# Kernel optimization log

Hardware: AMD Instinct MI355X
Metric: run time of the kernel (lower is better)

The kernel has to match this reference:

```python
import jax, jax.numpy as jnp
import numpy as np
import math

N_EMBD = 384
N_HEAD = 6
HEAD_DIM = N_EMBD // N_HEAD  # 64
EPS = 1e-5


def apply_rotary_emb(x, cos, sin):
    # x: [B, T, H, D]; cos/sin: [1, T, 1, D//2]
    d = x.shape[3] // 2
    x1, x2 = x[..., :d], x[..., d:]
    y1 = x1 * cos + x2 * sin
    y2 = -x1 * sin + x2 * cos
    return jnp.concatenate([y1, y2], axis=3).astype(x.dtype)


def rms_norm(x):
    # no learned gain, eps inside the sqrt's argument as in the torch code
    return x * jax.lax.rsqrt(jnp.mean(x * x, axis=-1, keepdims=True) + EPS)


def setup_inputs() -> dict:
    key = jax.random.key(0)
    ks = jax.random.split(key, 7)
    B, T = 8, 2048
    x = jax.random.normal(ks[0], (B, T, N_EMBD), dtype=jnp.float32)
    scale = 1.0 / math.sqrt(N_EMBD)
    Wq = jax.random.normal(ks[1], (N_EMBD, N_EMBD), dtype=jnp.float32) * scale
    Wk = jax.random.normal(ks[2], (N_EMBD, N_EMBD), dtype=jnp.float32) * scale
    Wv = jax.random.normal(ks[3], (N_EMBD, N_EMBD), dtype=jnp.float32) * scale
    Wo = jax.random.normal(ks[4], (N_EMBD, N_EMBD), dtype=jnp.float32) * scale
    # RoPE tables: true cos/sin of position*inv_freq
    half = HEAD_DIM // 2
    inv_freq = 1.0 / (10000.0 ** (jnp.arange(half, dtype=jnp.float32) / half))
    t = jnp.arange(T, dtype=jnp.float32)
    freqs = t[:, None] * inv_freq[None, :]  # [T, half]
    cos = jnp.cos(freqs)[None, :, None, :]  # [1, T, 1, half]
    sin = jnp.sin(freqs)[None, :, None, :]
    return {"x": x, "Wq": Wq, "Wk": Wk, "Wv": Wv, "Wo": Wo, "cos": cos, "sin": sin}


def reference(x, Wq, Wk, Wv, Wo, cos, sin):
    B, T, C = x.shape
    H, D = N_HEAD, HEAD_DIM
    # torch Linear: y = x @ W.T (weights stored [out, in])
    q = (x @ Wq.T).reshape(B, T, H, D)
    k = (x @ Wk.T).reshape(B, T, H, D)
    v = (x @ Wv.T).reshape(B, T, H, D)
    q = apply_rotary_emb(q, cos, sin)
    k = apply_rotary_emb(k, cos, sin)
    q = rms_norm(q)
    k = rms_norm(k)
    # attention: [B, H, T, T] scores, full softmax (no causal mask in source)
    att = jnp.einsum("bthd,bshd->bhts", q, k) * (1.0 / math.sqrt(D))
    att = jax.nn.softmax(att, axis=-1)
    y = jnp.einsum("bhts,bshd->bthd", att, v).reshape(B, T, C)
    return y @ Wo.T
```

## Files before the change

kernel.cpp:

```cpp
#include <hip/hip_runtime.h>
#include <hip/hip_bf16.h>
#include <stdint.h>

#define B_ 8
#define T_ 2048
#define C_ 384
#define H_ 6
#define D_ 64
#define M_ (B_*T_)

typedef unsigned short u16;
typedef unsigned int u32;
typedef __attribute__((ext_vector_type(8))) short short8;
typedef __attribute__((ext_vector_type(4))) float floatx4;
typedef __attribute__((ext_vector_type(16))) float floatx16;

#define QSCALE 0.18033688011112042f

__device__ __forceinline__ u16 f2b(float f) {
  union { float f; unsigned u; } x; x.f = f;
  unsigned r = x.u + 0x7fffu + ((x.u >> 16) & 1u);
  return (u16)(r >> 16);
}
__device__ __forceinline__ u32 pack_bf16(float a, float b) {
  union { __hip_bfloat162 h; u32 u; } x;
  x.h = __float22bfloat162_rn(float2{a, b});
  return x.u;
}
__device__ __forceinline__ uint4 pack8(const float4& lo, const float4& hi) {
  uint4 r;
  r.x = pack_bf16(lo.x, lo.y); r.y = pack_bf16(lo.z, lo.w);
  r.z = pack_bf16(hi.x, hi.y); r.w = pack_bf16(hi.z, hi.w);
  return r;
}

__device__ __forceinline__ void plswap(u32& a, u32& b) {
  asm("v_permlane32_swap_b32 %0, %1" : "+v"(a), "+v"(b));
}

__device__ __forceinline__ float fexp2(float x) {
#if __has_builtin(__builtin_amdgcn_exp2f)
  return __builtin_amdgcn_exp2f(x);
#else
  float r; asm("v_exp_f32 %0, %1" : "=v"(r) : "v"(x)); return r;
#endif
}

__device__ __forceinline__ u32 cvtpk(float a, float b) {
  u32 r; asm("v_cvt_pk_bf16_f32 %0, %1, %2" : "=v"(r) : "v"(a), "v"(b)); return r;
}

__device__ __forceinline__ void gl_lds16(const u16* g, u16* l) {
#if __has_builtin(__builtin_amdgcn_global_load_lds)
  __builtin_amdgcn_global_load_lds(
      (const __attribute__((address_space(1))) unsigned int*)g,
      (__attribute__((address_space(3))) unsigned int*)l,
      16, 0, 0);
#else
  *reinterpret_cast<uint4*>(l + (threadIdx.x & 63) * 8) =
      *reinterpret_cast<const uint4*>(g);
#endif
}

__global__ __launch_bounds__(256) void prep_bf16(
    const float* __restrict__ x,
    const float* __restrict__ wq, const float* __restrict__ wk,
    const float* __restrict__ wv, const float* __restrict__ wo,
    u16* __restrict__ xb,
    u16* __restrict__ wqb, u16* __restrict__ wkb,
    u16* __restrict__ wvb, u16* __restrict__ wob)
{
  const int c = blockIdx.x * 256 + threadIdx.x;
  const float* src;
  u16* dst;
  int off;
  if (c < 786432) {
    src = x; dst = xb; off = c;
  } else {
    int t = c - 786432;
    int wsel = t / 18432;
    off = t - wsel * 18432;
    src = (wsel == 0) ? wq : (wsel == 1) ? wk : (wsel == 2) ? wv : wo;
    dst = (wsel == 0) ? wqb : (wsel == 1) ? wkb : (wsel == 2) ? wvb : wob;
  }
  const float4* p = reinterpret_cast<const float4*>(src + (size_t)off * 8);
  float4 lo = p[0], hi = p[1];
  *reinterpret_cast<uint4*>(dst + (size_t)off * 8) = pack8(lo, hi);
}

#define QKV_SBUF 20480

__global__ __launch_bounds__(256) void qkv_fused(
    const u16* __restrict__ Xb,
    const u16* __restrict__ Wqb, const u16* __restrict__ Wkb, const u16* __restrict__ Wvb,
    const float* __restrict__ cosb, const float* __restrict__ sinb,
    u16* __restrict__ Qo, u16* __restrict__ Ko, u16* __restrict__ Vto)
{
  __shared__ __align__(16) u16 smem[2 * QKV_SBUF];

  const int id = blockIdx.x;
  const int xcd = id & 7;
  const int s = id >> 3;
  const int mb = xcd * 16 + s / 6;
  const int hh = s % 6;
  const int m0 = mb * 128;
  const int n0 = hh * 64;

  const int tid = threadIdx.x;
  const int w = tid >> 6;
  const int lane = tid & 63;
  const int quad = lane >> 4;
  const int c = lane & 15;

  const u16* Wz[3] = {Wqb, Wkb, Wvb};

  floatx4 acc[3][2][4];
#pragma unroll
  for (int z = 0; z < 3; z++)
#pragma unroll
    for (int i = 0; i < 2; i++)
#pragma unroll
      for (int j = 0; j < 4; j++) acc[z][i][j] = (floatx4){0.f, 0.f, 0.f, 0.f};

  const int lrow = lane >> 3;
  const int lcol = (lane & 7) * 8;

  auto STAGE = [&](int bb, int k0) {
    u16* base = smem + bb * QKV_SBUF;
#pragma unroll
    for (int n = 0; n < 4; n++) {
      const int ch = w * 4 + n;
      gl_lds16(Xb + (size_t)(m0 + ch * 8 + lrow) * C_ + k0 + lcol, base + ch * 512);
    }
#pragma unroll
    for (int z = 0; z < 3; z++)
#pragma unroll
      for (int n = 0; n < 2; n++) {
        const int ch = w * 2 + n;
        gl_lds16(Wz[z] + (size_t)(n0 + ch * 8 + lrow) * C_ + k0 + lcol,
                 base + 8192 + z * 4096 + ch * 512);
      }
  };

  STAGE(0, 0);
  __syncthreads();

  for (int i = 0; i < 6; i++) {
    const int bb = i & 1;
    if (i < 5) STAGE(bb ^ 1, (i + 1) * 64);

    const u16* As = smem + bb * QKV_SBUF;
    const u16* Bs0 = As + 8192;
#pragma unroll
    for (int ks = 0; ks < 2; ks++) {
      short8 af2[2];
#pragma unroll
      for (int mi = 0; mi < 2; mi++)
        af2[mi] = *reinterpret_cast<const short8*>(
            As + (w * 32 + mi * 16 + c) * 64 + (ks * 4 + quad) * 8);
#pragma unroll
      for (int z = 0; z < 3; z++) {
#pragma unroll
        for (int ni = 0; ni < 4; ni++) {
          short8 bf = *reinterpret_cast<const short8*>(
              Bs0 + z * 4096 + (ni * 16 + c) * 64 + (ks * 4 + quad) * 8);
#pragma unroll
          for (int mi = 0; mi < 2; mi++)
            acc[z][mi][ni] = __builtin_amdgcn_mfma_f32_16x16x32_bf16(af2[mi], bf, acc[z][mi][ni], 0, 0, 0);
        }
      }
    }
    if (i < 5) __syncthreads();
  }

  const int bb2 = m0 >> 11;
  const int tbase = m0 & (T_ - 1);

  {
    const size_t vbase = ((size_t)(bb2 * H_ + hh)) * D_ * T_;
#pragma unroll
    for (int mi = 0; mi < 2; mi++) {
      int t = tbase + w * 32 + mi * 16 + quad * 4;
#pragma unroll
      for (int ni = 0; ni < 4; ni++) {
        int d = ni * 16 + c;
        ushort4 pk;
        pk.x = f2b(acc[2][mi][ni][0]); pk.y = f2b(acc[2][mi][ni][1]);
        pk.z = f2b(acc[2][mi][ni][2]); pk.w = f2b(acc[2][mi][ni][3]);
        *reinterpret_cast<ushort4*>(Vto + vbase + (size_t)d * T_ + t) = pk;
      }
    }
  }

  u16* Ep = smem;
#pragma unroll
  for (int zz = 0; zz < 2; zz++) {
    __syncthreads();
#pragma unroll
    for (int mi = 0; mi < 2; mi++) {
      float ssr[4];
#pragma unroll
      for (int r = 0; r < 4; r++) {
        float s0 = acc[zz][mi][0][r], s1 = acc[zz][mi][1][r];
        float s2 = acc[zz][mi][2][r], s3 = acc[zz][mi][3][r];
        ssr[r] = s0 * s0 + s1 * s1 + s2 * s2 + s3 * s3;
      }
#pragma unroll
      for (int off = 1; off < 16; off <<= 1)
#pragma unroll
        for (int r = 0; r < 4; r++) ssr[r] += __shfl_xor(ssr[r], off, 64);
      int rowb = w * 32 + mi * 16 + quad * 4;
#pragma unroll
      for (int r = 0; r < 4; r++) {
        float scl = rsqrtf(ssr[r] * (1.0f / 64.0f) + 1e-5f);
        if (zz == 0) scl *= QSCALE;
        int t = tbase + rowb + r;
#pragma unroll
        for (int h2 = 0; h2 < 2; h2++) {
          float cs = cosb[t * 32 + h2 * 16 + c];
          float sn = sinb[t * 32 + h2 * 16 + c];
          float x1 = acc[zz][mi][h2][r];
          float x2 = acc[zz][mi][h2 + 2][r];
          Ep[(rowb + r) * 72 + h2 * 16 + c]       = f2b((x1 * cs + x2 * sn) * scl);
          Ep[(rowb + r) * 72 + (h2 + 2) * 16 + c] = f2b((x2 * cs - x1 * sn) * scl);
        }
      }
    }
    __syncthreads();
    {
      int row = tid >> 1, half = tid & 1;
      int t = tbase + row;
      u16* Og = (zz == 0) ? Qo : Ko;
      u16* dst = Og + (((size_t)(bb2 * H_ + hh)) * T_ + t) * D_ + half * 32;
#pragma unroll
      for (int i = 0; i < 4; i++)
        *reinterpret_cast<uint4*>(dst + i * 8) =
            *reinterpret_cast<const uint4*>(Ep + row * 72 + half * 32 + i * 8);
    }
  }
}

__global__ __launch_bounds__(256, 3) void attn_mfma(
    const u16* __restrict__ Qg, const u16* __restrict__ Kg,
    const u16* __restrict__ Vtg, u16* __restrict__ Yg)
{
  __shared__ __align__(16) u16 smem[16384];

  const int tid = threadIdx.x;
  const int w = tid >> 6;
  const int lane = tid & 63;
  const int hi = lane >> 5;
  const int lq = lane & 31;

  const int id = blockIdx.x;
  const int xcd = id & 7;
  const int slot = id >> 3;
  const int bh = xcd * 6 + (slot >> 4);
  const int q0 = (slot & 15) * 128;

  const size_t baseQK = (size_t)bh * T_ * D_;
  const size_t baseV  = (size_t)bh * D_ * T_;

  short8 qf[4];
  {
    const u16* qp = Qg + baseQK + (size_t)(q0 + w * 32 + lq) * D_ + hi * 8;
#pragma unroll
    for (int d = 0; d < 4; d++)
      qf[d] = *reinterpret_cast<const short8*>(qp + d * 16);
  }

  floatx16 z16;
#pragma unroll
  for (int i = 0; i < 16; i++) z16[i] = 0.f;

  const int sr = tid >> 2;
  const int sch = tid & 3;
  const int r3s = ((sr & 3) << 1) | ((sr >> 2) & 1);
  const int ko0 = sr * 64 + ((sch ^ r3s) * 8);
  const int ko1 = sr * 64 + (((sch + 4) ^ r3s) * 8);
  const int vo0 = 4096 + ko0;
  const int vo1 = 4096 + ko1;
  const u16* kga = Kg + baseQK + (size_t)sr * D_ + sch * 8;
  const u16* vga = Vtg + baseV + (size_t)sr * T_ + sch * 8;

  uint4 ka = *reinterpret_cast<const uint4*>(kga);
  uint4 kb = *reinterpret_cast<const uint4*>(kga + 32);
  uint4 va = *reinterpret_cast<const uint4*>(vga);
  uint4 vb = *reinterpret_cast<const uint4*>(vga + 32);
  *reinterpret_cast<uint4*>(smem + ko0) = ka;
  *reinterpret_cast<uint4*>(smem + ko1) = kb;
  *reinterpret_cast<uint4*>(smem + vo0) = va;
  *reinterpret_cast<uint4*>(smem + vo1) = vb;
  const u16* kload = kga + (size_t)64 * D_;
  const u16* vload = vga + 64;
  ka = *reinterpret_cast<const uint4*>(kload);
  kb = *reinterpret_cast<const uint4*>(kload + 32);
  va = *reinterpret_cast<const uint4*>(vload);
  vb = *reinterpret_cast<const uint4*>(vload + 32);
  kload += (size_t)64 * D_;
  vload += 64;

  floatx16 o0 = z16, o1 = z16;
  float l_part = 0.0f;

  const int r3q = ((lq & 3) << 1) | ((lq >> 2) & 1);

  int koff[2][4], voff[2][4];
#pragma unroll
  for (int ds = 0; ds < 4; ds++) {
    const int xr = (ds * 2 + hi) ^ r3q;
    koff[0][ds] = lq * 64 + xr * 8;
    koff[1][ds] = (32 + lq) * 64 + xr * 8;
    voff[0][ds] = 4096 + lq * 64 + xr * 8;
    voff[1][ds] = 4096 + (32 + lq) * 64 + xr * 8;
  }

  for (int kt = 0; kt < 32; kt++) {
    __syncthreads();

    const u16* Ksb = smem + ((kt & 1) << 13);

    floatx16 st0, st1;
    __builtin_amdgcn_s_setprio(1);
    {
      short8 kf0 = *reinterpret_cast<const short8*>(Ksb + koff[0][0]);
      short8 kf1 = *reinterpret_cast<const short8*>(Ksb + koff[1][0]);
      st0 = __builtin_amdgcn_mfma_f32_32x32x16_bf16(kf0, qf[0], z16, 0, 0, 0);
      st1 = __builtin_amdgcn_mfma_f32_32x32x16_bf16(kf1, qf[0], z16, 0, 0, 0);
    }
#pragma unroll
    for (int ds = 1; ds < 4; ds++) {
      short8 kf0 = *reinterpret_cast<const short8*>(Ksb + koff[0][ds]);
      short8 kf1 = *reinterpret_cast<const short8*>(Ksb + koff[1][ds]);
      st0 = __builtin_amdgcn_mfma_f32_32x32x16_bf16(kf0, qf[ds], st0, 0, 0, 0);
      st1 = __builtin_amdgcn_mfma_f32_32x32x16_bf16(kf1, qf[ds], st1, 0, 0, 0);
    }
    __builtin_amdgcn_s_setprio(0);

    if (kt < 31) {
      u16* wb = smem + (((kt + 1) & 1) << 13);
      *reinterpret_cast<uint4*>(wb + ko0) = ka;
      *reinterpret_cast<uint4*>(wb + ko1) = kb;
      *reinterpret_cast<uint4*>(wb + vo0) = va;
      *reinterpret_cast<uint4*>(wb + vo1) = vb;
      if (kt < 30) {
        ka = *reinterpret_cast<const uint4*>(kload);
        kb = *reinterpret_cast<const uint4*>(kload + 32);
        va = *reinterpret_cast<const uint4*>(vload);
        vb = *reinterpret_cast<const uint4*>(vload + 32);
        kload += (size_t)64 * D_;
        vload += 64;
      }
    }

#pragma unroll
    for (int r = 0; r < 16; r++) {
      float p0 = fexp2(st0[r]);
      float p1 = fexp2(st1[r]);
      st0[r] = p0;
      st1[r] = p1;
      l_part += p0 + p1;
    }

    short8 pa[4];
#pragma unroll
    for (int ks = 0; ks < 4; ks++) {
      const floatx16& s = (ks < 2) ? st0 : st1;
      const int rb = (ks & 1) * 8;
      u32 ca = cvtpk(s[rb + 0], s[rb + 1]);
      u32 cb = cvtpk(s[rb + 2], s[rb + 3]);
      u32 cc = cvtpk(s[rb + 4], s[rb + 5]);
      u32 cd = cvtpk(s[rb + 6], s[rb + 7]);
      plswap(ca, cc);
      plswap(cb, cd);
      short8 pf;
      u32* pfu = reinterpret_cast<u32*>(&pf);
      pfu[0] = ca; pfu[1] = cb; pfu[2] = cc; pfu[3] = cd;
      pa[ks] = pf;
    }

    __builtin_amdgcn_s_setprio(1);
#pragma unroll
    for (int ks = 0; ks < 4; ks++) {
      short8 vf0 = *reinterpret_cast<const short8*>(Ksb + voff[0][ks]);
      short8 vf1 = *reinterpret_cast<const short8*>(Ksb + voff[1][ks]);
      o0 = __builtin_amdgcn_mfma_f32_32x32x16_bf16(pa[ks], vf0, o0, 0, 0, 0);
      o1 = __builtin_amdgcn_mfma_f32_32x32x16_bf16(pa[ks], vf1, o1, 0, 0, 0);
    }
    __builtin_amdgcn_s_setprio(0);
  }

  float l_full = l_part + __shfl_xor(l_part, 32, 64);
  float inv = __builtin_amdgcn_rcpf(l_full);

  float invr[16];
#pragma unroll
  for (int r = 0; r < 16; r++) {
    const int qr = (r & 3) + 8 * (r >> 2) + 4 * hi;
    invr[r] = __shfl(inv, qr, 64);
  }

  __syncthreads();
  u16* Ep = smem + w * (32 * 72);
#pragma unroll
  for (int nt = 0; nt < 2; nt++) {
    const floatx16& o = nt ? o1 : o0;
#pragma unroll
    for (int r = 0; r < 16; r++) {
      const int rl = (r & 3) + 8 * (r >> 2) + 4 * hi;
      Ep[rl * 72 + nt * 32 + lq] = f2b(o[r] * invr[r]);
    }
  }
  __syncthreads();
  {
    const int row = tid >> 1, half = tid & 1;
    const u16* src = smem + (row >> 5) * (32 * 72) + (row & 31) * 72 + half * 32;
    const int t = q0 + row;
    const int b = bh / H_, h = bh % H_;
    const size_t yi = ((size_t)b * T_ + t) * C_ + (size_t)h * 64 + half * 32;
#pragma unroll
    for (int i = 0; i < 4; i++)
      *reinterpret_cast<uint4*>(Yg + yi + i * 8) =
          *reinterpret_cast<const uint4*>(src + i * 8);
  }
}

#define OUT_SBUF 12288

__global__ __launch_bounds__(256) void out_mfma(
    const u16* __restrict__ Xb, const u16* __restrict__ Wfb, float* __restrict__ Og)
{
  __shared__ __align__(16) u16 smem[2 * OUT_SBUF];

  const int id = blockIdx.x;
  const int xcd = id & 7;
  const int s = id >> 3;
  const int m0 = (xcd * 16 + s / 6) * 128;
  const int n0 = (s % 6) * 64;

  const int tid = threadIdx.x;
  const int w = tid >> 6;
  const int lane = tid & 63;
  const int quad = lane >> 4;
  const int c = lane & 15;

  floatx4 acc[2][4];
#pragma unroll
  for (int i = 0; i < 2; i++)
#pragma unroll
    for (int j = 0; j < 4; j++) acc[i][j] = (floatx4){0.f, 0.f, 0.f, 0.f};

  const int lrow = lane >> 3;
  const int lcol = (lane & 7) * 8;

  auto STAGE = [&](int bb, int k0) {
    u16* base = smem + bb * OUT_SBUF;
#pragma unroll
    for (int n = 0; n < 4; n++) {
      const int ch = w * 4 + n;
      gl_lds16(Xb + (size_t)(m0 + ch * 8 + lrow) * C_ + k0 + lcol, base + ch * 512);
    }
#pragma unroll
    for (int n = 0; n < 2; n++) {
      const int ch = w * 2 + n;
      gl_lds16(Wfb + (size_t)(n0 + ch * 8 + lrow) * C_ + k0 + lcol,
               base + 8192 + ch * 512);
    }
  };

  STAGE(0, 0);
  __syncthreads();

  for (int i = 0; i < 6; i++) {
    const int bb = i & 1;
    if (i < 5) STAGE(bb ^ 1, (i + 1) * 64);

    const u16* As = smem + bb * OUT_SBUF;
    const u16* Bs = As + 8192;
#pragma unroll
    for (int ks = 0; ks < 2; ks++) {
      short8 af[2], bf[4];
#pragma unroll
      for (int mi = 0; mi < 2; mi++)
        af[mi] = *reinterpret_cast<const short8*>(
            As + (w * 32 + mi * 16 + c) * 64 + (ks * 4 + quad) * 8);
#pragma unroll
      for (int ni = 0; ni < 4; ni++)
        bf[ni] = *reinterpret_cast<const short8*>(
            Bs + (ni * 16 + c) * 64 + (ks * 4 + quad) * 8);
#pragma unroll
      for (int mi = 0; mi < 2; mi++)
#pragma unroll
        for (int ni = 0; ni < 4; ni++)
          acc[mi][ni] = __builtin_amdgcn_mfma_f32_16x16x32_bf16(af[mi], bf[ni], acc[mi][ni], 0, 0, 0);
    }
    if (i < 5) __syncthreads();
  }

  __syncthreads();
  float* Ep = reinterpret_cast<float*>(smem) + w * (32 * 68);
#pragma unroll
  for (int mi = 0; mi < 2; mi++)
#pragma unroll
    for (int ni = 0; ni < 4; ni++) {
      int rw = mi * 16 + quad * 4;
      int col = ni * 16 + c;
#pragma unroll
      for (int r = 0; r < 4; r++)
        Ep[(rw + r) * 68 + col] = acc[mi][ni][r];
    }
  __syncthreads();
  {
    int rw2 = lane >> 1, half = lane & 1;
    const float* src = Ep + rw2 * 68 + half * 32;
    float* dst = Og + (size_t)(m0 + w * 32 + rw2) * C_ + n0 + half * 32;
#pragma unroll
    for (int i = 0; i < 8; i++)
      *reinterpret_cast<float4*>(dst + i * 4) =
          *reinterpret_cast<const float4*>(src + i * 4);
  }
}

extern "C" void kernel_launch(void* const* d_in, const int* in_sizes, int n_in,
                              void* d_out, int out_size, void* d_ws, size_t ws_size,
                              hipStream_t stream) {
  (void)in_sizes; (void)n_in; (void)out_size; (void)ws_size;
  const float* x    = (const float*)d_in[0];
  const float* Wq   = (const float*)d_in[1];
  const float* Wk   = (const float*)d_in[2];
  const float* Wv   = (const float*)d_in[3];
  const float* Wo   = (const float*)d_in[4];
  const float* cosb = (const float*)d_in[5];
  const float* sinb = (const float*)d_in[6];

  const size_t MC = (size_t)M_ * C_;
  u16* ws = (u16*)d_ws;
  u16* Q   = ws;
  u16* K   = Q + MC;
  u16* Vt  = K + MC;
  u16* Y   = Vt + MC;
  u16* Xb  = Y;
  u16* Wb  = Y + MC;
  u16* Wqb = Wb;
  u16* Wkb = Wb + 147456;
  u16* Wvb = Wb + 2 * 147456;
  u16* Wob = Wb + 3 * 147456;
  float* out = (float*)d_out;

  prep_bf16<<<3360, 256, 0, stream>>>(x, Wq, Wk, Wv, Wo, Xb, Wqb, Wkb, Wvb, Wob);

  qkv_fused<<<768, 256, 0, stream>>>(Xb, Wqb, Wkb, Wvb, cosb, sinb, Q, K, Vt);

  attn_mfma<<<768, 256, 0, stream>>>(Q, K, Vt, Y);

  out_mfma<<<768, 256, 0, stream>>>(Y, Wob, out);
}
```

Before: 206.2 us.

## Process two 32-row query tiles per warp in attention to reuse K/V fragments

```diff
diff --git a/kernel.cpp b/kernel.cpp
--- a/kernel.cpp
+++ b/kernel.cpp
@@ -240,7 +240,7 @@
   }
 }
 
-__global__ __launch_bounds__(256, 3) void attn_mfma(
+__global__ __launch_bounds__(256, 2) void attn_mfma(
     const u16* __restrict__ Qg, const u16* __restrict__ Kg,
     const u16* __restrict__ Vtg, u16* __restrict__ Yg)
 {
@@ -255,18 +255,20 @@
   const int id = blockIdx.x;
   const int xcd = id & 7;
   const int slot = id >> 3;
-  const int bh = xcd * 6 + (slot >> 4);
-  const int q0 = (slot & 15) * 128;
+  const int bh = xcd * 6 + (slot >> 3);
+  const int q0 = (slot & 7) * 256;
 
   const size_t baseQK = (size_t)bh * T_ * D_;
   const size_t baseV  = (size_t)bh * D_ * T_;
 
-  short8 qf[4];
+  short8 qfA[4], qfB[4];
   {
-    const u16* qp = Qg + baseQK + (size_t)(q0 + w * 32 + lq) * D_ + hi * 8;
-#pragma unroll
-    for (int d = 0; d < 4; d++)
-      qf[d] = *reinterpret_cast<const short8*>(qp + d * 16);
+    const u16* qp = Qg + baseQK + (size_t)(q0 + w * 64 + lq) * D_ + hi * 8;
+#pragma unroll
+    for (int d = 0; d < 4; d++) {
+      qfA[d] = *reinterpret_cast<const short8*>(qp + d * 16);
+      qfB[d] = *reinterpret_cast<const short8*>(qp + (size_t)32 * D_ + d * 16);
+    }
   }
 
   floatx16 z16;
@@ -300,8 +302,8 @@
   kload += (size_t)64 * D_;
   vload += 64;
 
-  floatx16 o0 = z16, o1 = z16;
-  float l_part = 0.0f;
+  floatx16 oA0 = z16, oA1 = z16, oB0 = z16, oB1 = z16;
+  float lA0 = 0.f, lA1 = 0.f, lB0 = 0.f, lB1 = 0.f;
 
   const int r3q = ((lq & 3) << 1) | ((lq >> 2) & 1);
 
@@ -317,25 +319,6 @@
 
   for (int kt = 0; kt < 32; kt++) {
     __syncthreads();
-
-    const u16* Ksb = smem + ((kt & 1) << 13);
-
-    floatx16 st0, st1;
-    __builtin_amdgcn_s_setprio(1);
-    {
-      short8 kf0 = *reinterpret_cast<const short8*>(Ksb + koff[0][0]);
-      short8 kf1 = *reinterpret_cast<const short8*>(Ksb + koff[1][0]);
-      st0 = __builtin_amdgcn_mfma_f32_32x32x16_bf16(kf0, qf[0], z16, 0, 0, 0);
-      st1 = __builtin_amdgcn_mfma_f32_32x32x16_bf16(kf1, qf[0], z16, 0, 0, 0);
-    }
-#pragma unroll
-    for (int ds = 1; ds < 4; ds++) {
-      short8 kf0 = *reinterpret_cast<const short8*>(Ksb + koff[0][ds]);
-      short8 kf1 = *reinterpret_cast<const short8*>(Ksb + koff[1][ds]);
-      st0 = __builtin_amdgcn_mfma_f32_32x32x16_bf16(kf0, qf[ds], st0, 0, 0, 0);
-      st1 = __builtin_amdgcn_mfma_f32_32x32x16_bf16(kf1, qf[ds], st1, 0, 0, 0);
-    }
-    __builtin_amdgcn_s_setprio(0);
 
     if (kt < 31) {
       u16* wb = smem + (((kt + 1) & 1) << 13);
@@ -353,16 +336,34 @@
       }
     }
 
+    const u16* Ksb = smem + ((kt & 1) << 13);
+
+    short8 kreg0[4], kreg1[4];
+    floatx16 st0, st1;
+    __builtin_amdgcn_s_setprio(1);
+    {
+      kreg0[0] = *reinterpret_cast<const short8*>(Ksb + koff[0][0]);
+      kreg1[0] = *reinterpret_cast<const short8*>(Ksb + koff[1][0]);
+      st0 = __builtin_amdgcn_mfma_f32_32x32x16_bf16(kreg0[0], qfA[0], z16, 0, 0, 0);
+      st1 = __builtin_amdgcn_mfma_f32_32x32x16_bf16(kreg1[0], qfA[0], z16, 0, 0, 0);
+    }
+#pragma unroll
+    for (int ds = 1; ds < 4; ds++) {
+      kreg0[ds] = *reinterpret_cast<const short8*>(Ksb + koff[0][ds]);
+      kreg1[ds] = *reinterpret_cast<const short8*>(Ksb + koff[1][ds]);
+      st0 = __builtin_amdgcn_mfma_f32_32x32x16_bf16(kreg0[ds], qfA[ds], st0, 0, 0, 0);
+      st1 = __builtin_amdgcn_mfma_f32_32x32x16_bf16(kreg1[ds], qfA[ds], st1, 0, 0, 0);
+    }
+    __builtin_amdgcn_s_setprio(0);
+
 #pragma unroll
     for (int r = 0; r < 16; r++) {
       float p0 = fexp2(st0[r]);
       float p1 = fexp2(st1[r]);
-      st0[r] = p0;
-      st1[r] = p1;
-      l_part += p0 + p1;
-    }
-
-    short8 pa[4];
+      st0[r] = p0; st1[r] = p1;
+      lA0 += p0; lA1 += p1;
+    }
+    short8 paA[4];
 #pragma unroll
     for (int ks = 0; ks < 4; ks++) {
       const floatx16& s = (ks < 2) ? st0 : st1;
@@ -376,7 +377,41 @@
       short8 pf;
       u32* pfu = reinterpret_cast<u32*>(&pf);
       pfu[0] = ca; pfu[1] = cb; pfu[2] = cc; pfu[3] = cd;
-      pa[ks] = pf;
+      paA[ks] = pf;
+    }
+
+    __builtin_amdgcn_s_setprio(1);
+    st0 = __builtin_amdgcn_mfma_f32_32x32x16_bf16(kreg0[0], qfB[0], z16, 0, 0, 0);
+    st1 = __builtin_amdgcn_mfma_f32_32x32x16_bf16(kreg1[0], qfB[0], z16, 0, 0, 0);
+#pragma unroll
+    for (int ds = 1; ds < 4; ds++) {
+      st0 = __builtin_amdgcn_mfma_f32_32x32x16_bf16(kreg0[ds], qfB[ds], st0, 0, 0, 0);
+      st1 = __builtin_amdgcn_mfma_f32_32x32x16_bf16(kreg1[ds], qfB[ds], st1, 0, 0, 0);
+    }
+    __builtin_amdgcn_s_setprio(0);
+
+#pragma unroll
+    for (int r = 0; r < 16; r++) {
+      float p0 = fexp2(st0[r]);
+      float p1 = fexp2(st1[r]);
+      st0[r] = p0; st1[r] = p1;
+      lB0 += p0; lB1 += p1;
+    }
+    short8 paB[4];
+#pragma unroll
+    for (int ks = 0; ks < 4; ks++) {
+      const floatx16& s = (ks < 2) ? st0 : st1;
+      const int rb = (ks & 1) * 8;
+      u32 ca = cvtpk(s[rb + 0], s[rb + 1]);
+      u32 cb = cvtpk(s[rb + 2], s[rb + 3]);
+      u32 cc = cvtpk(s[rb + 4], s[rb + 5]);
+      u32 cd = cvtpk(s[rb + 6], s[rb + 7]);
+      plswap(ca, cc);
+      plswap(cb, cd);
+      short8 pf;
+      u32* pfu = reinterpret_cast<u32*>(&pf);
+      pfu[0] = ca; pfu[1] = cb; pfu[2] = cc; pfu[3] = cd;
+      paB[ks] = pf;
     }
 
     __builtin_amdgcn_s_setprio(1);
@@ -384,44 +419,56 @@
     for (int ks = 0; ks < 4; ks++) {
       short8 vf0 = *reinterpret_cast<const short8*>(Ksb + voff[0][ks]);
       short8 vf1 = *reinterpret_cast<const short8*>(Ksb + voff[1][ks]);
-      o0 = __builtin_amdgcn_mfma_f32_32x32x16_bf16(pa[ks], vf0, o0, 0, 0, 0);
-      o1 = __builtin_amdgcn_mfma_f32_32x32x16_bf16(pa[ks], vf1, o1, 0, 0, 0);
+      oA0 = __builtin_amdgcn_mfma_f32_32x32x16_bf16(paA[ks], vf0, oA0, 0, 0, 0);
+      oA1 = __builtin_amdgcn_mfma_f32_32x32x16_bf16(paA[ks], vf1, oA1, 0, 0, 0);
+      oB0 = __builtin_amdgcn_mfma_f32_32x32x16_bf16(paB[ks], vf0, oB0, 0, 0, 0);
+      oB1 = __builtin_amdgcn_mfma_f32_32x32x16_bf16(paB[ks], vf1, oB1, 0, 0, 0);
     }
     __builtin_amdgcn_s_setprio(0);
   }
 
-  float l_full = l_part + __shfl_xor(l_part, 32, 64);
-  float inv = __builtin_amdgcn_rcpf(l_full);
-
-  float invr[16];
+  float lA = lA0 + lA1;
+  float lB = lB0 + lB1;
+  lA += __shfl_xor(lA, 32, 64);
+  lB += __shfl_xor(lB, 32, 64);
+  float invA = __builtin_amdgcn_rcpf(lA);
+  float invB = __builtin_amdgcn_rcpf(lB);
+  float invrA[16], invrB[16];
 #pragma unroll
   for (int r = 0; r < 16; r++) {
     const int qr = (r & 3) + 8 * (r >> 2) + 4 * hi;
-    invr[r] = __shfl(inv, qr, 64);
-  }
-
-  __syncthreads();
-  u16* Ep = smem + w * (32 * 72);
-#pragma unroll
-  for (int nt = 0; nt < 2; nt++) {
-    const floatx16& o = nt ? o1 : o0;
-#pragma unroll
-    for (int r = 0; r < 16; r++) {
-      const int rl = (r & 3) + 8 * (r >> 2) + 4 * hi;
-      Ep[rl * 72 + nt * 32 + lq] = f2b(o[r] * invr[r]);
-    }
-  }
-  __syncthreads();
-  {
-    const int row = tid >> 1, half = tid & 1;
-    const u16* src = smem + (row >> 5) * (32 * 72) + (row & 31) * 72 + half * 32;
-    const int t = q0 + row;
-    const int b = bh / H_, h = bh % H_;
-    const size_t yi = ((size_t)b * T_ + t) * C_ + (size_t)h * 64 + half * 32;
-#pragma unroll
-    for (int i = 0; i < 4; i++)
-      *reinterpret_cast<uint4*>(Yg + yi + i * 8) =
-          *reinterpret_cast<const uint4*>(src + i * 8);
+    invrA[r] = __shfl(invA, qr, 64);
+    invrB[r] = __shfl(invB, qr, 64);
+  }
+
+  const int b = bh / H_, h = bh % H_;
+#pragma unroll
+  for (int pass = 0; pass < 2; pass++) {
+    __syncthreads();
+    u16* Ep = smem + w * (32 * 72);
+    const floatx16& p0 = pass ? oB0 : oA0;
+    const floatx16& p1 = pass ? oB1 : oA1;
+    const float* ivr = pass ? invrB : invrA;
+#pragma unroll
+    for (int nt = 0; nt < 2; nt++) {
+      const floatx16& o = nt ? p1 : p0;
+#pragma unroll
+      for (int r = 0; r < 16; r++) {
+        const int rl = (r & 3) + 8 * (r >> 2) + 4 * hi;
+        Ep[rl * 72 + nt * 32 + lq] = f2b(o[r] * ivr[r]);
+      }
+    }
+    __syncthreads();
+    {
+      const int row = tid >> 1, half = tid & 1;
+      const u16* src = smem + (row >> 5) * (32 * 72) + (row & 31) * 72 + half * 32;
+      const int t = q0 + (row >> 5) * 64 + pass * 32 + (row & 31);
+      const size_t yi = ((size_t)b * T_ + t) * C_ + (size_t)h * 64 + half * 32;
+#pragma unroll
+      for (int i = 0; i < 4; i++)
+        *reinterpret_cast<uint4*>(Yg + yi + i * 8) =
+            *reinterpret_cast<const uint4*>(src + i * 8);
+    }
   }
 }
 
@@ -551,7 +598,7 @@
 
   qkv_fused<<<768, 256, 0, stream>>>(Xb, Wqb, Wkb, Wvb, cosb, sinb, Q, K, Vt);
 
-  attn_mfma<<<768, 256, 0, stream>>>(Q, K, Vt, Y);
+  attn_mfma<<<384, 256, 0, stream>>>(Q, K, Vt, Y);
 
   out_mfma<<<768, 256, 0, stream>>>(Y, Wob, out);
 }
```

Result: slower. 213.2 us (+3.4%).
